# Kernel tuning notes

Measured on AMD Instinct MI355X. Metric: run time of the kernel, lower is better.

Reference implementation:

```python
import jax, jax.numpy as jnp
import numpy as np

# module hyperparameters (from init_kwargs)
R_MIN, R_MAX = 0.01, 0.6
RH, RW = 64, 64          # retinal_H, retinal_W
H, W = 64, 128           # output pooled H, W
UFR, UFT = 4, 4          # upsampling factors


def make_grid(weight):
    """Vectorized version of get_grid. weight: [B,2].
    Faithful to source: only the top-left [H, W] corner of the
    [H*UFR, W*UFT] grid is written; the rest (torch.empty in the
    original) is set to 0 here for determinism."""
    i = jnp.arange(H, dtype=jnp.float32)
    j = jnp.arange(W, dtype=jnp.float32)
    xg = (i - (H // 2)) / (H / 2.0)
    yg = (j - (W // 2)) / (W / 2.0)
    xx, yy = jnp.meshgrid(xg, yg, indexing="ij")  # [H,W]
    # clamp radius to avoid log(0) = -inf at the center pixel; the resulting
    # coordinate is far out of [-1,1] and gets border-clamped either way.
    logr = jnp.log(jnp.maximum(jnp.sqrt(xx ** 2 + yy ** 2), 1e-12))  # [H,W]
    lo = jnp.log(weight[:, 0] * R_MIN)[:, None, None]  # [B,1,1]
    hi = jnp.log(weight[:, 1] * R_MAX)[:, None, None]  # [B,1,1]
    r = RH * (logr[None] - lo) / (hi - lo)             # [B,H,W]
    a = jnp.arctan2(yy, xx)
    a = jnp.where(a > 0, a, 2.0 * np.pi + a)
    t = 0.5 * a * RW / np.pi                           # [H,W]
    gx = jnp.broadcast_to((t / (RW / 2.0) - 1.0)[None], r.shape)
    gy = r / (RH / 2.0) - 1.0
    small = jnp.stack([gx, gy], axis=-1)               # [B,H,W,2]
    grid = jnp.zeros((weight.shape[0], H * UFR, W * UFT, 2), jnp.float32)
    return grid.at[:, :H, :W, :].set(small)


def grid_sample_border(x, grid):
    """torch.F.grid_sample, mode=bilinear, padding_mode=border, align_corners=False.
    x: [B,C,Hin,Win], grid: [B,Hg,Wg,2] -> [B,C,Hg,Wg]."""
    B, C, Hin, Win = x.shape
    gx, gy = grid[..., 0], grid[..., 1]
    ix = jnp.clip(((gx + 1.0) * Win - 1.0) * 0.5, 0.0, Win - 1.0)
    iy = jnp.clip(((gy + 1.0) * Hin - 1.0) * 0.5, 0.0, Hin - 1.0)
    x0f = jnp.floor(ix)
    y0f = jnp.floor(iy)
    wx = (ix - x0f)[..., None]
    wy = (iy - y0f)[..., None]
    x0 = jnp.clip(x0f.astype(jnp.int32), 0, Win - 1)
    y0 = jnp.clip(y0f.astype(jnp.int32), 0, Hin - 1)
    x1 = jnp.clip(x0 + 1, 0, Win - 1)
    y1 = jnp.clip(y0 + 1, 0, Hin - 1)
    bidx = jnp.arange(B)[:, None, None]
    gather = lambda yi, xi: x[bidx, :, yi, xi]  # [B,Hg,Wg,C]
    out = (gather(y0, x0) * (1 - wx) * (1 - wy)
           + gather(y0, x1) * wx * (1 - wy)
           + gather(y1, x0) * (1 - wx) * wy
           + gather(y1, x1) * wx * wy)
    return jnp.transpose(out, (0, 3, 1, 2))  # [B,C,Hg,Wg]


def setup_inputs() -> dict:
    key = jax.random.key(0)
    k1, k2, k3, k4, k5, k6 = jax.random.split(key, 6)
    B, C, Hin, Win = 8, 64, 224, 224
    Cmid = C // 2  # int(channel * r)
    return {
        "x": jax.random.normal(k1, (B, C, Hin, Win), jnp.float32),
        "l_t_prev": jax.random.uniform(k2, (B, 2), jnp.float32),
        "w1": jax.random.normal(k3, (C, Cmid), jnp.float32) * 0.1,
        "b1": jnp.zeros((Cmid,), jnp.float32),
        "w2": jax.random.normal(k4, (Cmid, 2), jnp.float32) * 0.1,
        "b2": jnp.zeros((2,), jnp.float32),
    }


def reference(x, l_t_prev, w1, b1, w2, b2):
    # att: global avg pool -> fc -> sigmoid
    branch = x.mean(axis=(2, 3))                              # [B,C]
    weight = jax.nn.sigmoid(jax.nn.relu(branch @ w1 + b1) @ w2 + b2)  # [B,2]
    grid = make_grid(weight) + l_t_prev[:, None, None, :]     # [B,Hg,Wg,2]
    sampled = grid_sample_border(x, grid)                     # [B,C,Hg,Wg]
    B, C = sampled.shape[:2]
    pooled = sampled.reshape(B, C, H, UFR, W, UFT).mean(axis=(3, 5))  # AvgPool2d([UFR,UFT])
    return pooled, weight
```

## Files before the change

### kernel.cpp

```cpp
#include <hip/hip_runtime.h>
#include <math.h>

#define B 8
#define C 64
#define HIN 224
#define WIN 224
#define PLANE (HIN*WIN)
#define PLANE4 (PLANE/4)
#define QUART (PLANE4/4)
#define OH 64
#define OW 128
#define OUT_PER_BC (OH*OW)
#define POOLED_SIZE (B*C*OH*OW)

#define WS_PARTIAL 0

#define PI_F 3.14159265358979323846f

__device__ __forceinline__ float bilinear(const float* __restrict__ p,
                                          float ix, float iy) {
    float x0f = floorf(ix), y0f = floorf(iy);
    int x0 = (int)x0f, y0 = (int)y0f;
    float wx = ix - x0f, wy = iy - y0f;
    int x1 = min(x0 + 1, WIN - 1);
    int y1 = min(y0 + 1, HIN - 1);
    const float* r0 = p + y0 * WIN;
    const float* r1 = p + y1 * WIN;
    float v00 = r0[x0], v01 = r0[x1], v10 = r1[x0], v11 = r1[x1];
    float v0 = v00 + (v01 - v00) * wx;
    float v1 = v10 + (v11 - v10) * wx;
    return v0 + (v1 - v0) * wy;
}

__global__ __launch_bounds__(256) void k1_gap_fill(const float* __restrict__ x,
                                                   const float* __restrict__ l_t,
                                                   float* __restrict__ ws,
                                                   float* __restrict__ out) {
    int blk = blockIdx.x;
    int bc  = blk >> 2, q = blk & 3;
    int b   = bc >> 6;
    int tid = threadIdx.x;

    const float4* p = (const float4*)x + (size_t)bc * PLANE4 + q * QUART;
    float s = 0.f;
#pragma unroll
    for (int k = 0; k < 12; ++k) {
        float4 v = p[tid + k * 256];
        s += (v.x + v.y) + (v.z + v.w);
    }
    if (tid < QUART - 12 * 256) {
        float4 v = p[tid + 12 * 256];
        s += (v.x + v.y) + (v.z + v.w);
    }

    const float* plane = x + (size_t)bc * PLANE;
    float gx = l_t[b * 2 + 0], gy = l_t[b * 2 + 1];
    float ixc = fminf(fmaxf(((gx + 1.f) * (float)WIN - 1.f) * 0.5f, 0.f), (float)(WIN - 1));
    float iyc = fminf(fmaxf(((gy + 1.f) * (float)HIN - 1.f) * 0.5f, 0.f), (float)(HIN - 1));
    float vc = bilinear(plane, ixc, iyc);
    float4 vc4 = make_float4(vc, vc, vc, vc);

    float4* o4 = (float4*)(out + (size_t)bc * OUT_PER_BC);
    if (q == 0) {
#pragma unroll
        for (int k = 0; k < 2; ++k) {
            int f4i = tid + k * 256;
            if (f4i < 384) {
                int row = f4i / 24;
                int c4  = f4i - row * 24 + 8;
                o4[row * 32 + c4] = vc4;
            }
        }
    } else {
        o4[q * 512 + tid]       = vc4;
        o4[q * 512 + 256 + tid] = vc4;
    }

    for (int off = 32; off; off >>= 1) s += __shfl_down(s, off, 64);
    __shared__ float lds[4];
    if ((tid & 63) == 0) lds[tid >> 6] = s;
    __syncthreads();
    if (tid == 0) ws[WS_PARTIAL + blk] = lds[0] + lds[1] + lds[2] + lds[3];
}

__global__ __launch_bounds__(256) void k3_fused(const float* __restrict__ x,
                                                const float* __restrict__ w1,
                                                const float* __restrict__ b1,
                                                const float* __restrict__ w2,
                                                const float* __restrict__ b2,
                                                const float* __restrict__ l_t,
                                                const float* __restrict__ ws,
                                                float* __restrict__ out_weight,
                                                float* __restrict__ out) {
    int blk   = blockIdx.x;
    int bc    = blk >> 4;
    int patch = blk & 15;
    int b     = bc >> 6;
    int tid   = threadIdx.x;

    __shared__ float branch[C];
    __shared__ float hidden[32];
    __shared__ float sparams[4];

    if (tid < C) {
        const float* pp = ws + WS_PARTIAL + (b * C + tid) * 4;
        branch[tid] = (pp[0] + pp[1] + pp[2] + pp[3]) * (1.0f / PLANE);
    }
    __syncthreads();
    if (tid < 32) {
        float h = b1[tid];
        for (int c = 0; c < C; ++c) h += branch[c] * w1[c * 32 + tid];
        hidden[tid] = h > 0.f ? h : 0.f;
    }
    __syncthreads();
    if (tid < 2) {
        float sacc = b2[tid];
        for (int m = 0; m < 32; ++m) sacc += hidden[m] * w2[m * 2 + tid];
        float wv = 1.f / (1.f + expf(-sacc));
        if ((bc & 63) == 0 && patch == 0) out_weight[b * 2 + tid] = wv;
        sparams[tid]     = logf(wv * (tid == 0 ? 0.01f : 0.6f));
        sparams[2 + tid] = l_t[b * 2 + tid];
    }
    __syncthreads();

    float lo  = sparams[0], hi = sparams[1];
    float inv_hl = 1.f / (hi - lo);
    float ltx = sparams[2], lty = sparams[3];

    int wave   = tid >> 6;
    int lane   = tid & 63;
    int wave_h = wave >> 1;
    int wave_w = wave & 1;
    int fi_l   = lane >> 3;
    int fj_l   = lane & 7;

    int pb_h = patch >> 2;
    int pb_w = patch & 3;
    int fi   = pb_h * 16 + wave_h * 8 + fi_l;
    int fjb  = pb_w * 32 + wave_w * 16;
    int fj0  = fjb + fj_l;
    int fj1  = fjb + 8 + fj_l;

    float xg = (float)(fi - 32) * (1.f / 32.f);
    float ix0, iy0, ix1, iy1;
    {
        float yg = (float)(fj0 - 64) * (1.f / 64.f);
        float rr = sqrtf(xg * xg + yg * yg);
        float r  = 64.f * (logf(fmaxf(rr, 1e-12f)) - lo) * inv_hl;
        float a  = atan2f(yg, xg);
        if (!(a > 0.f)) a = 2.f * PI_F + a;
        float t  = a * (32.f / PI_F);
        float gxv = t * (1.f / 32.f) - 1.f + ltx;
        float gyv = r * (1.f / 32.f) - 1.f + lty;
        ix0 = fminf(fmaxf(((gxv + 1.f) * (float)WIN - 1.f) * 0.5f, 0.f), (float)(WIN - 1));
        iy0 = fminf(fmaxf(((gyv + 1.f) * (float)HIN - 1.f) * 0.5f, 0.f), (float)(HIN - 1));
    }
    {
        float yg = (float)(fj1 - 64) * (1.f / 64.f);
        float rr = sqrtf(xg * xg + yg * yg);
        float r  = 64.f * (logf(fmaxf(rr, 1e-12f)) - lo) * inv_hl;
        float a  = atan2f(yg, xg);
        if (!(a > 0.f)) a = 2.f * PI_F + a;
        float t  = a * (32.f / PI_F);
        float gxv = t * (1.f / 32.f) - 1.f + ltx;
        float gyv = r * (1.f / 32.f) - 1.f + lty;
        ix1 = fminf(fmaxf(((gxv + 1.f) * (float)WIN - 1.f) * 0.5f, 0.f), (float)(WIN - 1));
        iy1 = fminf(fmaxf(((gyv + 1.f) * (float)HIN - 1.f) * 0.5f, 0.f), (float)(HIN - 1));
    }

    const float* plane = x + (size_t)bc * PLANE;
    float a0 = bilinear(plane, ix0, iy0);
    float a1 = bilinear(plane, ix1, iy1);

    a0 += __shfl_xor(a0, 1, 64);  a1 += __shfl_xor(a1, 1, 64);
    a0 += __shfl_xor(a0, 2, 64);  a1 += __shfl_xor(a1, 2, 64);
    a0 += __shfl_xor(a0, 8, 64);  a1 += __shfl_xor(a1, 8, 64);
    a0 += __shfl_xor(a0, 16, 64); a1 += __shfl_xor(a1, 16, 64);

    if ((lane & 27) == 0) {
        int ph = pb_h * 4 + wave_h * 2 + (fi_l >> 2);
        int pw = pb_w * 8 + wave_w * 4 + (fj_l >> 2);
        float* o = out + (size_t)bc * OUT_PER_BC + ph * 128 + pw;
        o[0] = a0 * (1.f / 16.f);
        o[2] = a1 * (1.f / 16.f);
    }
}

extern "C" void kernel_launch(void* const* d_in, const int* in_sizes, int n_in,
                              void* d_out, int out_size, void* d_ws, size_t ws_size,
                              hipStream_t stream) {
    const float* x   = (const float*)d_in[0];
    const float* l_t = (const float*)d_in[1];
    const float* w1  = (const float*)d_in[2];
    const float* b1  = (const float*)d_in[3];
    const float* w2  = (const float*)d_in[4];
    const float* b2  = (const float*)d_in[5];
    float* out = (float*)d_out;
    float* ws  = (float*)d_ws;

    k1_gap_fill<<<dim3(B * C * 4), dim3(256), 0, stream>>>(x, l_t, ws, out);
    k3_fused<<<dim3(B * C * 16), dim3(256), 0, stream>>>(
        x, w1, b1, w2, b2, l_t, ws, out + POOLED_SIZE, out);
}
```

Before: 185.1 us.

## Share grid coordinates and MLP across 16 channels per block in sampling kernel

The sampling kernel now launches one block per (batch, patch, channel-group) and loops over 16 channels. The MLP, log/atan2 grid math and clamp are computed once and reused for every channel in the loop, and two channels are gathered per iteration to raise memory-level parallelism. The cost is a 16x smaller grid (512 blocks), which lowers occupancy and parallelism for the latency-bound gathers.

```diff
diff --git a/kernel.cpp b/kernel.cpp
--- a/kernel.cpp
+++ b/kernel.cpp
@@ -83,19 +83,20 @@
     if (tid == 0) ws[WS_PARTIAL + blk] = lds[0] + lds[1] + lds[2] + lds[3];
 }
 
-__global__ __launch_bounds__(256) void k3_fused(const float* __restrict__ x,
-                                                const float* __restrict__ w1,
-                                                const float* __restrict__ b1,
-                                                const float* __restrict__ w2,
-                                                const float* __restrict__ b2,
-                                                const float* __restrict__ l_t,
-                                                const float* __restrict__ ws,
-                                                float* __restrict__ out_weight,
-                                                float* __restrict__ out) {
+__global__ __launch_bounds__(256) void k3_combined(const float* __restrict__ x,
+                                                   const float* __restrict__ w1,
+                                                   const float* __restrict__ b1,
+                                                   const float* __restrict__ w2,
+                                                   const float* __restrict__ b2,
+                                                   const float* __restrict__ l_t,
+                                                   const float* __restrict__ ws,
+                                                   float* __restrict__ out_weight,
+                                                   float* __restrict__ out) {
     int blk   = blockIdx.x;
-    int bc    = blk >> 4;
-    int patch = blk & 15;
-    int b     = bc >> 6;
+    int b     = blk >> 6;
+    int g     = blk & 63;
+    int patch = g >> 2;
+    int cgrp  = g & 3;
     int tid   = threadIdx.x;
 
     __shared__ float branch[C];
@@ -117,13 +118,13 @@
         float sacc = b2[tid];
         for (int m = 0; m < 32; ++m) sacc += hidden[m] * w2[m * 2 + tid];
         float wv = 1.f / (1.f + expf(-sacc));
-        if ((bc & 63) == 0 && patch == 0) out_weight[b * 2 + tid] = wv;
+        if (g == 0) out_weight[b * 2 + tid] = wv;
         sparams[tid]     = logf(wv * (tid == 0 ? 0.01f : 0.6f));
         sparams[2 + tid] = l_t[b * 2 + tid];
     }
     __syncthreads();
 
-    float lo  = sparams[0], hi = sparams[1];
+    float lo = sparams[0], hi = sparams[1];
     float inv_hl = 1.f / (hi - lo);
     float ltx = sparams[2], lty = sparams[3];
 
@@ -149,8 +150,7 @@
         float r  = 64.f * (logf(fmaxf(rr, 1e-12f)) - lo) * inv_hl;
         float a  = atan2f(yg, xg);
         if (!(a > 0.f)) a = 2.f * PI_F + a;
-        float t  = a * (32.f / PI_F);
-        float gxv = t * (1.f / 32.f) - 1.f + ltx;
+        float gxv = a * (1.f / PI_F) - 1.f + ltx;
         float gyv = r * (1.f / 32.f) - 1.f + lty;
         ix0 = fminf(fmaxf(((gxv + 1.f) * (float)WIN - 1.f) * 0.5f, 0.f), (float)(WIN - 1));
         iy0 = fminf(fmaxf(((gyv + 1.f) * (float)HIN - 1.f) * 0.5f, 0.f), (float)(HIN - 1));
@@ -161,28 +161,44 @@
         float r  = 64.f * (logf(fmaxf(rr, 1e-12f)) - lo) * inv_hl;
         float a  = atan2f(yg, xg);
         if (!(a > 0.f)) a = 2.f * PI_F + a;
-        float t  = a * (32.f / PI_F);
-        float gxv = t * (1.f / 32.f) - 1.f + ltx;
+        float gxv = a * (1.f / PI_F) - 1.f + ltx;
         float gyv = r * (1.f / 32.f) - 1.f + lty;
         ix1 = fminf(fmaxf(((gxv + 1.f) * (float)WIN - 1.f) * 0.5f, 0.f), (float)(WIN - 1));
         iy1 = fminf(fmaxf(((gyv + 1.f) * (float)HIN - 1.f) * 0.5f, 0.f), (float)(HIN - 1));
     }
 
-    const float* plane = x + (size_t)bc * PLANE;
-    float a0 = bilinear(plane, ix0, iy0);
-    float a1 = bilinear(plane, ix1, iy1);
-
-    a0 += __shfl_xor(a0, 1, 64);  a1 += __shfl_xor(a1, 1, 64);
-    a0 += __shfl_xor(a0, 2, 64);  a1 += __shfl_xor(a1, 2, 64);
-    a0 += __shfl_xor(a0, 8, 64);  a1 += __shfl_xor(a1, 8, 64);
-    a0 += __shfl_xor(a0, 16, 64); a1 += __shfl_xor(a1, 16, 64);
-
-    if ((lane & 27) == 0) {
-        int ph = pb_h * 4 + wave_h * 2 + (fi_l >> 2);
-        int pw = pb_w * 8 + wave_w * 4 + (fj_l >> 2);
-        float* o = out + (size_t)bc * OUT_PER_BC + ph * 128 + pw;
-        o[0] = a0 * (1.f / 16.f);
-        o[2] = a1 * (1.f / 16.f);
+    bool writer = ((lane & 27) == 0);
+    int ph = pb_h * 4 + wave_h * 2 + (fi_l >> 2);
+    int pw = pb_w * 8 + wave_w * 4 + (fj_l >> 2);
+
+    int bc0 = b * C + cgrp * 16;
+    const float* plane = x + (size_t)bc0 * PLANE;
+    float* obase = out + (size_t)bc0 * OUT_PER_BC + ph * 128 + pw;
+
+#pragma unroll
+    for (int cc = 0; cc < 16; cc += 2) {
+        float a0 = bilinear(plane, ix0, iy0);
+        float a1 = bilinear(plane, ix1, iy1);
+        float b0 = bilinear(plane + PLANE, ix0, iy0);
+        float b1v = bilinear(plane + PLANE, ix1, iy1);
+
+        a0 += __shfl_xor(a0, 1, 64);  a1 += __shfl_xor(a1, 1, 64);
+        b0 += __shfl_xor(b0, 1, 64);  b1v += __shfl_xor(b1v, 1, 64);
+        a0 += __shfl_xor(a0, 2, 64);  a1 += __shfl_xor(a1, 2, 64);
+        b0 += __shfl_xor(b0, 2, 64);  b1v += __shfl_xor(b1v, 2, 64);
+        a0 += __shfl_xor(a0, 8, 64);  a1 += __shfl_xor(a1, 8, 64);
+        b0 += __shfl_xor(b0, 8, 64);  b1v += __shfl_xor(b1v, 8, 64);
+        a0 += __shfl_xor(a0, 16, 64); a1 += __shfl_xor(a1, 16, 64);
+        b0 += __shfl_xor(b0, 16, 64); b1v += __shfl_xor(b1v, 16, 64);
+
+        if (writer) {
+            obase[0] = a0 * (1.f / 16.f);
+            obase[2] = a1 * (1.f / 16.f);
+            obase[OUT_PER_BC]     = b0  * (1.f / 16.f);
+            obase[OUT_PER_BC + 2] = b1v * (1.f / 16.f);
+        }
+        plane += 2 * PLANE;
+        obase += 2 * OUT_PER_BC;
     }
 }
 
@@ -199,6 +215,6 @@
     float* ws  = (float*)d_ws;
 
     k1_gap_fill<<<dim3(B * C * 4), dim3(256), 0, stream>>>(x, l_t, ws, out);
-    k3_fused<<<dim3(B * C * 16), dim3(256), 0, stream>>>(
+    k3_combined<<<dim3(B * C), dim3(256), 0, stream>>>(
         x, w1, b1, w2, b2, l_t, ws, out + POOLED_SIZE, out);
 }
```

Result: faster. 173.8 us (-6.1%).
